# Kernel optimization log

Hardware: AMD Instinct MI355X
Metric: run time of the kernel (lower is better)

The kernel has to match this reference:

```python
import jax, jax.numpy as jnp
import numpy as np

B, C, H, W = 16, 128, 32, 32
D, K = 64, 8192
BN_EPS = 1e-5
KLD_SCALE = 10.0
COMMIT = 0.25


def setup_inputs() -> dict:
    key = jax.random.key(0)
    ks = jax.random.split(key, 4)
    return {
        "z": jax.random.normal(ks[0], (B, C, H, W), dtype=jnp.float32),
        "proj_w": jax.random.normal(ks[1], (D, C), dtype=jnp.float32) * (1.0 / np.sqrt(C)),
        "proj_b": jax.random.normal(ks[2], (D,), dtype=jnp.float32) * 0.01,
        "gamma": jnp.ones((D,), dtype=jnp.float32),
        "beta": jnp.zeros((D,), dtype=jnp.float32),
        "running_mean": jnp.zeros((D,), dtype=jnp.float32),
        "running_var": jnp.ones((D,), dtype=jnp.float32),
        "embed": jax.random.normal(ks[3], (K, D), dtype=jnp.float32) * 0.1,
    }


def reference(z, proj_w, proj_b, gamma, beta, running_mean, running_var, embed):
    sg = jax.lax.stop_gradient
    b, c, h, w = z.shape
    # 1x1 conv projection: [B,C,H,W] -> [B,D,H,W]
    x = jnp.einsum('bchw,dc->bdhw', z, proj_w) + proj_b[None, :, None, None]
    # BatchNorm2d (inference mode: running stats)
    scale = gamma * jax.lax.rsqrt(running_var + BN_EPS)
    x = x * scale[None, :, None, None] + (beta - running_mean * scale)[None, :, None, None]
    # NCHW -> NHWC, flatten to [N, D]
    z_e = jnp.transpose(x, (0, 2, 3, 1))
    flat = z_e.reshape(-1, z_e.shape[-1])  # [N, D]
    # pairwise squared distances [N, K]
    dist = (jnp.sum(flat * flat, axis=1, keepdims=True)
            - 2.0 * flat @ embed.T
            + jnp.sum(embed * embed, axis=1)[None, :])
    ind = jnp.argmax(-dist, axis=1).reshape(b, h, w)  # [B,H,W]
    z_q = embed[ind]  # [B,H,W,D] codebook gather
    diff = KLD_SCALE * (COMMIT * jnp.mean((sg(z_q) - z_e) ** 2)
                        + jnp.mean((z_q - sg(z_e)) ** 2))
    z_q_st = z_e + sg(z_q - z_e)  # straight-through
    return jnp.transpose(z_q_st, (0, 3, 1, 2)), diff, ind
```

## Files before the change

### kernel.cpp

```cpp
#include <hip/hip_runtime.h>
#include <math.h>

#define B_   16
#define C_   128
#define H_   32
#define W_   32
#define D_   64
#define K_   8192
#define HW_  (H_*W_)
#define N_   (B_*HW_)

#define CS      32
#define CPB     (K_/CS)
#define ROWS_PB 256
#define MARGIN  0.12f
#define CAND_CAP 32

typedef short v8s __attribute__((ext_vector_type(8)));
typedef float v4f __attribute__((ext_vector_type(4)));

__device__ __forceinline__ short f2bf(float f) {
    union { float fv; unsigned u; } cv; cv.fv = f;
    unsigned u = cv.u;
    unsigned rnd = ((u >> 16) & 1u) + 0x7fffu;
    return (short)((u + rnd) >> 16);
}

#define GLOAD_LDS16(gp, lp) __builtin_amdgcn_global_load_lds( \
    (const __attribute__((address_space(1))) unsigned int*)(gp), \
    (__attribute__((address_space(3))) unsigned int*)(lp), 16, 0, 0)

__device__ __forceinline__ float exact_score(const float4* __restrict__ zr,
                                             const float* __restrict__ embed,
                                             float h, int k)
{
    const float4* ep = (const float4*)(embed + (size_t)k * D_);
    float sa = 0.f, sb = 0.f;
    #pragma unroll
    for (int d4 = 0; d4 < 16; d4 += 2) {
        float4 ea = ep[d4], eb = ep[d4 + 1];
        sa += ea.x*zr[d4].x + ea.y*zr[d4].y + ea.z*zr[d4].z + ea.w*zr[d4].w;
        sb += eb.x*zr[d4+1].x + eb.y*zr[d4+1].y + eb.z*zr[d4+1].z + eb.w*zr[d4+1].w;
    }
    return (sa + sb) - h;
}

__global__ __launch_bounds__(256) void k_projprep(
    const float* __restrict__ z, const float* __restrict__ pw,
    const float* __restrict__ pb, const float* __restrict__ gamma,
    const float* __restrict__ beta, const float* __restrict__ rmean,
    const float* __restrict__ rvar, const float* __restrict__ embed,
    float* __restrict__ ze, short* __restrict__ zbfT,
    short* __restrict__ ebs, float* __restrict__ hn)
{
    __shared__ float zt[128][64];
    __shared__ float wl[64][128];
    const int tid = threadIdx.x;

    if (blockIdx.x >= 256) {
        int t = (blockIdx.x - 256) * 256 + tid;
        float4 v = ((const float4*)embed)[t];
        float s = v.x*v.x + v.y*v.y + v.z*v.z + v.w*v.w;
        s += __shfl_xor(s, 1);
        s += __shfl_xor(s, 2);
        s += __shfl_xor(s, 4);
        s += __shfl_xor(s, 8);
        const int k = t >> 4, p = t & 15;
        if (p == 0) hn[k] = 0.5f * s;
        if (p < 8) {
            const int j = p ^ (k & 7);
            const float* src = embed + (size_t)k * D_ + j * 8;
            v8s o;
            #pragma unroll
            for (int i = 0; i < 8; ++i) o[i] = f2bf(src[i]);
            *(v8s*)(ebs + (size_t)k * D_ + p * 8) = o;
        }
        return;
    }

    const int n0  = blockIdx.x * 64;
    const int b   = n0 / HW_;
    const int hw0 = n0 % HW_;
    const float* zb = z + (size_t)b * C_ * HW_ + hw0;

    #pragma unroll
    for (int it = 0; it < 8; ++it) {
        int flat = tid + 256 * it;
        int c = flat >> 4, p4 = flat & 15;
        *(float4*)&zt[c][4*p4] = *(const float4*)&zb[c * HW_ + 4*p4];
    }
    #pragma unroll
    for (int it = 0; it < 8; ++it) {
        int flat = tid + 256 * it;
        int d = flat >> 5, c4i = flat & 31;
        *(float4*)&wl[d][4*c4i] = *(const float4*)&pw[d * C_ + 4*c4i];
    }
    __syncthreads();

    const int tp = tid & 15;
    const int td = tid >> 4;
    float acc[4][4] = {};
    #pragma unroll
    for (int c4 = 0; c4 < 32; ++c4) {
        float4 zq[4], wv[4];
        #pragma unroll
        for (int k = 0; k < 4; ++k) zq[k] = *(const float4*)&zt[4*c4 + k][4*tp];
        #pragma unroll
        for (int j = 0; j < 4; ++j) wv[j] = *(const float4*)&wl[4*td + j][4*c4];
        #pragma unroll
        for (int i = 0; i < 4; ++i)
            #pragma unroll
            for (int j = 0; j < 4; ++j)
                acc[i][j] += zq[0][i]*wv[j].x + zq[1][i]*wv[j].y
                           + zq[2][i]*wv[j].z + zq[3][i]*wv[j].w;
    }

    float sc[4], bi[4];
    #pragma unroll
    for (int j = 0; j < 4; ++j) {
        int d = 4*td + j;
        float s = gamma[d] / sqrtf(rvar[d] + 1e-5f);
        sc[j] = s;
        bi[j] = pb[d] * s + beta[d] - rmean[d] * s;
    }
    short* tbase = zbfT + (size_t)blockIdx.x * 4096;
    const int islot_base = (tp >> 2) * 2 + (td >> 3);
    const int lane_hi    = ((td >> 1) & 3) * 16;
    const int el0        = 4 * (td & 1);
    #pragma unroll
    for (int i = 0; i < 4; ++i) {
        int n = n0 + 4*tp + i;
        float4 o;
        o.x = acc[i][0]*sc[0] + bi[0];
        o.y = acc[i][1]*sc[1] + bi[1];
        o.z = acc[i][2]*sc[2] + bi[2];
        o.w = acc[i][3]*sc[3] + bi[3];
        *(float4*)&ze[(size_t)n * D_ + 4*td] = o;
        short4 ob;
        ob.x = f2bf(o.x); ob.y = f2bf(o.y); ob.z = f2bf(o.z); ob.w = f2bf(o.w);
        const int lane = lane_hi + ((4*tp + i) & 15);
        *(short4*)(tbase + islot_base * 512 + lane * 8 + el0) = ob;
    }
}

template<bool PUSH>
__global__ __launch_bounds__(256) void k_sweep(
    const short* __restrict__ zbfT, const short* __restrict__ ebs,
    const float* __restrict__ hn, float* __restrict__ pbest,
    const float* __restrict__ Vm, int* __restrict__ cnt,
    int* __restrict__ cand)
{
    __shared__ short eb[CPB * 64];
    __shared__ float hl[CPB];
    const int tid  = threadIdx.x;
    const int lane = tid & 63;
    const int wv   = tid >> 6;
    const int q    = lane >> 4;
    const int l15  = lane & 15;
    const int m8   = l15 & 7;
    const int rowBase = blockIdx.x * ROWS_PB + wv * 64;
    const int code0   = blockIdx.y * CPB;

    {
        const char* s_ = (const char*)(ebs + (size_t)code0 * 64);
        char* l_ = (char*)&eb[0];
        #pragma unroll
        for (int i = 0; i < 8; ++i) {
            int seg = (wv * 8 + i) * 1024 + lane * 16;
            GLOAD_LDS16(s_ + seg, l_ + seg);
        }
        hl[tid] = hn[code0 + tid];
    }

    const short* aw = zbfT + (size_t)(blockIdx.x * 4 + wv) * 4096;
    v8s A[4][2];
    #pragma unroll
    for (int i = 0; i < 8; ++i)
        A[i >> 1][i & 1] = *(const v8s*)(aw + i * 512 + lane * 8);

    float best[4][4];
    float vm[4][4];
    if (PUSH) {
        #pragma unroll
        for (int rt = 0; rt < 4; ++rt)
            #pragma unroll
            for (int r = 0; r < 4; ++r)
                vm[rt][r] = Vm[rowBase + rt*16 + q*4 + r];
    } else {
        #pragma unroll
        for (int rt = 0; rt < 4; ++rt)
            #pragma unroll
            for (int r = 0; r < 4; ++r) best[rt][r] = -INFINITY;
    }

    const int rb0 = l15 * 64 + ((q ^ m8) * 8);
    const int rb1 = l15 * 64 + (((q ^ m8) ^ 4) * 8);

    __syncthreads();

    #pragma unroll 1
    for (int tc = 0; tc < 2; ++tc) {
        #pragma unroll
        for (int ti = 0; ti < 8; ++ti) {
            const int t = tc * 8 + ti;
            v8s B0 = *(const v8s*)(&eb[0] + rb0 + t * 1024);
            v8s B1 = *(const v8s*)(&eb[0] + rb1 + t * 1024);
            const float mh = -hl[t * 16 + l15];
            #pragma unroll
            for (int rt = 0; rt < 4; ++rt) {
                v4f c = {mh, mh, mh, mh};
                c = __builtin_amdgcn_mfma_f32_16x16x32_bf16(A[rt][0], B0, c, 0, 0, 0);
                c = __builtin_amdgcn_mfma_f32_16x16x32_bf16(A[rt][1], B1, c, 0, 0, 0);
                if (!PUSH) {
                    #pragma unroll
                    for (int r = 0; r < 4; ++r) best[rt][r] = fmaxf(best[rt][r], c[r]);
                } else {
                    bool a0 = c[0] > vm[rt][0];
                    bool a1 = c[1] > vm[rt][1];
                    bool a2 = c[2] > vm[rt][2];
                    bool a3 = c[3] > vm[rt][3];
                    if (a0 | a1 | a2 | a3) {
                        const int code = code0 + t * 16 + l15;
                        const int row0 = rowBase + rt*16 + q*4;
                        #pragma unroll
                        for (int r = 0; r < 4; ++r) {
                            if (c[r] > vm[rt][r]) {
                                int s = atomicAdd(&cnt[row0 + r], 1);
                                if (s < CAND_CAP) cand[(row0 + r) * CAND_CAP + s] = code;
                            }
                        }
                    }
                }
            }
        }
    }

    if (!PUSH) {
        #pragma unroll
        for (int rt = 0; rt < 4; ++rt)
            #pragma unroll
            for (int r = 0; r < 4; ++r) {
                float v = best[rt][r];
                v = fmaxf(v, __shfl_xor(v, 1));
                v = fmaxf(v, __shfl_xor(v, 2));
                v = fmaxf(v, __shfl_xor(v, 4));
                v = fmaxf(v, __shfl_xor(v, 8));
                if (l15 == 0)
                    pbest[(size_t)blockIdx.y * N_ + rowBase + rt*16 + q*4 + r] = v;
            }
    }
}

__global__ __launch_bounds__(256) void k_comb(const float* __restrict__ pbest,
                                              float* __restrict__ Vm,
                                              int* __restrict__ cnt,
                                              float* __restrict__ outDiff)
{
    int n = blockIdx.x * 256 + threadIdx.x;
    float v = -INFINITY;
    #pragma unroll
    for (int s = 0; s < CS; ++s) v = fmaxf(v, pbest[(size_t)s * N_ + n]);
    Vm[n] = v - MARGIN;
    cnt[n] = 0;
    if (n == 0) *outDiff = 0.f;
}

__global__ __launch_bounds__(64) void k_pick(
    const int* __restrict__ cnt, const int* __restrict__ cand,
    const float* __restrict__ embed, const float* __restrict__ hn,
    const float* __restrict__ ze, float* __restrict__ out0,
    float* __restrict__ outIdx, float* __restrict__ outDiff)
{
    const int tid = threadIdx.x;
    const int n   = blockIdx.x * 64 + tid;

    float4 zr[16];
    const float4* zp = (const float4*)(ze + (size_t)n * D_);
    #pragma unroll
    for (int i = 0; i < 16; ++i) zr[i] = zp[i];

    const int m = cnt[n];
    float best = -INFINITY;
    int   bidx = 0x7fffffff;
    if (m == 0 || m > CAND_CAP) {
        for (int k = 0; k < K_; ++k) {
            float s = exact_score(zr, embed, hn[k], k);
            if (s > best) { best = s; bidx = k; }
        }
    } else {
        for (int i = 0; i < m; ++i) {
            int k = cand[n * CAND_CAP + i];
            float s = exact_score(zr, embed, hn[k], k);
            if (s > best || (s == best && k < bidx)) { best = s; bidx = k; }
        }
    }
    if (bidx == 0x7fffffff) bidx = 0;
    outIdx[n] = (float)bidx;

    const float4* eq = (const float4*)(embed + (size_t)bidx * D_);
    const int b = n >> 10, hw = n & 1023;
    float* o = out0 + (size_t)b * (D_ * HW_) + hw;

    float local = 0.f;
    #pragma unroll
    for (int d4 = 0; d4 < 16; ++d4) {
        float4 e = eq[d4], zv = zr[d4];
        float dx = e.x - zv.x, dy = e.y - zv.y, dz = e.z - zv.z, dw = e.w - zv.w;
        local += dx*dx + dy*dy + dz*dz + dw*dw;
        o[(4*d4 + 0) * HW_] = e.x;
        o[(4*d4 + 1) * HW_] = e.y;
        o[(4*d4 + 2) * HW_] = e.z;
        o[(4*d4 + 3) * HW_] = e.w;
    }

    local += __shfl_xor(local, 1);
    local += __shfl_xor(local, 2);
    local += __shfl_xor(local, 4);
    local += __shfl_xor(local, 8);
    local += __shfl_xor(local, 16);
    local += __shfl_xor(local, 32);
    if (tid == 0) atomicAdd(outDiff, local * (12.5f / (float)(N_ * D_)));
}

extern "C" void kernel_launch(void* const* d_in, const int* in_sizes, int n_in,
                              void* d_out, int out_size, void* d_ws, size_t ws_size,
                              hipStream_t stream)
{
    const float* z     = (const float*)d_in[0];
    const float* pw    = (const float*)d_in[1];
    const float* pb    = (const float*)d_in[2];
    const float* gamma = (const float*)d_in[3];
    const float* beta  = (const float*)d_in[4];
    const float* rmean = (const float*)d_in[5];
    const float* rvar  = (const float*)d_in[6];
    const float* embed = (const float*)d_in[7];

    float* out = (float*)d_out;
    float* out0    = out;
    float* outDiff = out + (size_t)N_ * D_;
    float* outIdx  = outDiff + 1;

    float* ws    = (float*)d_ws;
    float* ze    = ws;
    short* zbfT  = (short*)(ze + (size_t)N_ * D_);
    short* ebs   = zbfT + (size_t)N_ * D_;
    float* hn    = (float*)(ebs + (size_t)K_ * D_);
    float* pbest = hn + K_;
    float* Vm    = pbest + (size_t)CS * N_;
    int*   cnt   = (int*)(Vm + N_);
    int*   cand  = cnt + N_;

    k_projprep<<<256 + 512, 256, 0, stream>>>(z, pw, pb, gamma, beta, rmean,
                                              rvar, embed, ze, zbfT, ebs, hn);
    k_sweep<false><<<dim3(N_ / ROWS_PB, CS), 256, 0, stream>>>(
        zbfT, ebs, hn, pbest, nullptr, nullptr, nullptr);
    k_comb <<<N_ / 256, 256, 0, stream>>>(pbest, Vm, cnt, outDiff);
    k_sweep<true><<<dim3(N_ / ROWS_PB, CS), 256, 0, stream>>>(
        zbfT, ebs, hn, pbest, Vm, cnt, cand);
    k_pick <<<N_ / 64, 64, 0, stream>>>(cnt, cand, embed, hn, ze, out0,
                                        outIdx, outDiff);
}
```

Measured before the change: 157.6 us.

## Fuse combine kernel into push sweep and double sweep block rows

```diff
diff --git a/kernel.cpp b/kernel.cpp
--- a/kernel.cpp
+++ b/kernel.cpp
@@ -12,7 +12,7 @@
 
 #define CS      32
 #define CPB     (K_/CS)
-#define ROWS_PB 256
+#define ROWS_PB 512
 #define MARGIN  0.12f
 #define CAND_CAP 32
 
@@ -51,14 +51,16 @@
     const float* __restrict__ beta, const float* __restrict__ rmean,
     const float* __restrict__ rvar, const float* __restrict__ embed,
     float* __restrict__ ze, short* __restrict__ zbfT,
-    short* __restrict__ ebs, float* __restrict__ hn)
+    short* __restrict__ ebs, float* __restrict__ hn,
+    int* __restrict__ cnt, float* __restrict__ outDiff)
 {
     __shared__ float zt[128][64];
     __shared__ float wl[64][128];
     const int tid = threadIdx.x;
 
     if (blockIdx.x >= 256) {
-        int t = (blockIdx.x - 256) * 256 + tid;
+        const int pbk = blockIdx.x - 256;
+        int t = pbk * 256 + tid;
         float4 v = ((const float4*)embed)[t];
         float s = v.x*v.x + v.y*v.y + v.z*v.z + v.w*v.w;
         s += __shfl_xor(s, 1);
@@ -75,6 +77,8 @@
             for (int i = 0; i < 8; ++i) o[i] = f2bf(src[i]);
             *(v8s*)(ebs + (size_t)k * D_ + p * 8) = o;
         }
+        if (pbk < 64) cnt[pbk * 256 + tid] = 0;
+        if (pbk == 0 && tid == 0) *outDiff = 0.f;
         return;
     }
 
@@ -144,14 +148,14 @@
 }
 
 template<bool PUSH>
-__global__ __launch_bounds__(256) void k_sweep(
+__global__ __launch_bounds__(512) void k_sweep(
     const short* __restrict__ zbfT, const short* __restrict__ ebs,
     const float* __restrict__ hn, float* __restrict__ pbest,
-    const float* __restrict__ Vm, int* __restrict__ cnt,
-    int* __restrict__ cand)
+    int* __restrict__ cnt, int* __restrict__ cand)
 {
     __shared__ short eb[CPB * 64];
     __shared__ float hl[CPB];
+    __shared__ float vml[ROWS_PB];
     const int tid  = threadIdx.x;
     const int lane = tid & 63;
     const int wv   = tid >> 6;
@@ -165,18 +169,31 @@
         const char* s_ = (const char*)(ebs + (size_t)code0 * 64);
         char* l_ = (char*)&eb[0];
         #pragma unroll
-        for (int i = 0; i < 8; ++i) {
-            int seg = (wv * 8 + i) * 1024 + lane * 16;
+        for (int i = 0; i < 4; ++i) {
+            int seg = (wv * 4 + i) * 1024 + lane * 16;
             GLOAD_LDS16(s_ + seg, l_ + seg);
         }
-        hl[tid] = hn[code0 + tid];
-    }
-
-    const short* aw = zbfT + (size_t)(blockIdx.x * 4 + wv) * 4096;
+        if (tid < CPB) hl[tid] = hn[code0 + tid];
+    }
+
+    if (PUSH) {
+        float v = -INFINITY;
+        const int row = blockIdx.x * ROWS_PB + tid;
+        #pragma unroll
+        for (int s = 0; s < CS; ++s) v = fmaxf(v, pbest[(size_t)s * N_ + row]);
+        vml[tid] = v - MARGIN;
+    }
+
+    const short* aw = zbfT + (size_t)(blockIdx.x * 8 + wv) * 4096;
     v8s A[4][2];
     #pragma unroll
     for (int i = 0; i < 8; ++i)
         A[i >> 1][i & 1] = *(const v8s*)(aw + i * 512 + lane * 8);
+
+    const int rb0 = l15 * 64 + ((q ^ m8) * 8);
+    const int rb1 = l15 * 64 + (((q ^ m8) ^ 4) * 8);
+
+    __syncthreads();
 
     float best[4][4];
     float vm[4][4];
@@ -185,18 +202,13 @@
         for (int rt = 0; rt < 4; ++rt)
             #pragma unroll
             for (int r = 0; r < 4; ++r)
-                vm[rt][r] = Vm[rowBase + rt*16 + q*4 + r];
+                vm[rt][r] = vml[wv * 64 + rt*16 + q*4 + r];
     } else {
         #pragma unroll
         for (int rt = 0; rt < 4; ++rt)
             #pragma unroll
             for (int r = 0; r < 4; ++r) best[rt][r] = -INFINITY;
     }
-
-    const int rb0 = l15 * 64 + ((q ^ m8) * 8);
-    const int rb1 = l15 * 64 + (((q ^ m8) ^ 4) * 8);
-
-    __syncthreads();
 
     #pragma unroll 1
     for (int tc = 0; tc < 2; ++tc) {
@@ -251,20 +263,6 @@
     }
 }
 
-__global__ __launch_bounds__(256) void k_comb(const float* __restrict__ pbest,
-                                              float* __restrict__ Vm,
-                                              int* __restrict__ cnt,
-                                              float* __restrict__ outDiff)
-{
-    int n = blockIdx.x * 256 + threadIdx.x;
-    float v = -INFINITY;
-    #pragma unroll
-    for (int s = 0; s < CS; ++s) v = fmaxf(v, pbest[(size_t)s * N_ + n]);
-    Vm[n] = v - MARGIN;
-    cnt[n] = 0;
-    if (n == 0) *outDiff = 0.f;
-}
-
 __global__ __launch_bounds__(64) void k_pick(
     const int* __restrict__ cnt, const int* __restrict__ cand,
     const float* __restrict__ embed, const float* __restrict__ hn,
@@ -346,17 +344,16 @@
     short* ebs   = zbfT + (size_t)N_ * D_;
     float* hn    = (float*)(ebs + (size_t)K_ * D_);
     float* pbest = hn + K_;
-    float* Vm    = pbest + (size_t)CS * N_;
-    int*   cnt   = (int*)(Vm + N_);
+    int*   cnt   = (int*)(pbest + (size_t)CS * N_);
     int*   cand  = cnt + N_;
 
     k_projprep<<<256 + 512, 256, 0, stream>>>(z, pw, pb, gamma, beta, rmean,
-                                              rvar, embed, ze, zbfT, ebs, hn);
-    k_sweep<false><<<dim3(N_ / ROWS_PB, CS), 256, 0, stream>>>(
-        zbfT, ebs, hn, pbest, nullptr, nullptr, nullptr);
-    k_comb <<<N_ / 256, 256, 0, stream>>>(pbest, Vm, cnt, outDiff);
-    k_sweep<true><<<dim3(N_ / ROWS_PB, CS), 256, 0, stream>>>(
-        zbfT, ebs, hn, pbest, Vm, cnt, cand);
+                                              rvar, embed, ze, zbfT, ebs, hn,
+                                              cnt, outDiff);
+    k_sweep<false><<<dim3(N_ / ROWS_PB, CS), 512, 0, stream>>>(
+        zbfT, ebs, hn, pbest, nullptr, nullptr);
+    k_sweep<true><<<dim3(N_ / ROWS_PB, CS), 512, 0, stream>>>(
+        zbfT, ebs, hn, pbest, cnt, cand);
     k_pick <<<N_ / 64, 64, 0, stream>>>(cnt, cand, embed, hn, ze, out0,
                                         outIdx, outDiff);
 }
```

Measured after the change: 148.0 us, median of 2. 6.1% less time.
